# Optimization experiments

Measured on AMD Instinct MI355X. Metric: run time of the kernel, lower is better.

The kernel has to match this reference:

```python
import jax, jax.numpy as jnp
import numpy as np

N, E, H = 40000, 320000, 128
T = 4                      # towers
F_IN = H // T              # 32, divide_input=True
F_OUT = H // T             # 32
NUM_AGG, NUM_SCALER = 5, 3


def _lin(k, out_d, in_d):
    return jax.random.normal(k, (out_d, in_d), jnp.float32) / np.sqrt(in_d)


def setup_inputs() -> dict:
    key = jax.random.key(0)
    ks = jax.random.split(key, 16)
    inp = {}
    inp["atom_x"] = jax.random.normal(ks[0], (N, H), jnp.float32)
    inp["bond_x"] = jax.random.randint(ks[1], (E,), 0, 5)
    inp["atom_edge_index"] = jax.random.randint(ks[2], (2, E), 0, N)
    inp["deg_hist"] = jnp.ones((17,), jnp.int32)
    # bond embedding table (Embedding(5, H))
    inp["emb"] = jax.random.normal(ks[3], (5, H), jnp.float32)
    # edge_encoder: Linear(edge_dim=H, F_IN)
    inp["edge_w"] = _lin(ks[4], F_IN, H)
    inp["edge_b"] = jnp.zeros((F_IN,), jnp.float32)
    # pre_nns per tower: Linear(3F,F) -> ReLU -> Linear(F,F)
    inp["pre_w0"] = jax.random.normal(ks[5], (T, F_IN, 3 * F_IN), jnp.float32) / np.sqrt(3 * F_IN)
    inp["pre_b0"] = jnp.zeros((T, F_IN), jnp.float32)
    inp["pre_w1"] = jax.random.normal(ks[6], (T, F_IN, F_IN), jnp.float32) / np.sqrt(F_IN)
    inp["pre_b1"] = jnp.zeros((T, F_IN), jnp.float32)
    # post_nns per tower: Linear((5*3+1)F, F) -> ReLU -> Linear(F,F)
    post_in = (NUM_AGG * NUM_SCALER + 1) * F_IN
    inp["post_w0"] = jax.random.normal(ks[7], (T, F_OUT, post_in), jnp.float32) / np.sqrt(post_in)
    inp["post_b0"] = jnp.zeros((T, F_OUT), jnp.float32)
    inp["post_w1"] = jax.random.normal(ks[8], (T, F_OUT, F_OUT), jnp.float32) / np.sqrt(F_OUT)
    inp["post_b1"] = jnp.zeros((T, F_OUT), jnp.float32)
    # final Linear(H, H)
    inp["lin_w"] = _lin(ks[9], H, H)
    inp["lin_b"] = jnp.zeros((H,), jnp.float32)
    # LayerNorm(H)
    inp["ln_g"] = jnp.ones((H,), jnp.float32)
    inp["ln_b"] = jnp.zeros((H,), jnp.float32)
    return inp


def _pna_forward(atom_x, bond_emb, src, dst, deg_hist,
                 edge_w, edge_b, pre_w0, pre_b0, pre_w1, pre_b1,
                 post_w0, post_b0, post_w1, post_b1, lin_w, lin_b, ln_g, ln_b):
    n = atom_x.shape[0]
    x = atom_x.reshape(n, T, F_IN)                       # divide_input
    # message: cat([x_i, x_j, edge_attr]) per tower, then per-tower pre-MLP
    e = bond_emb @ edge_w.T + edge_b                     # [E, F_IN]
    e = jnp.broadcast_to(e[:, None, :], (e.shape[0], T, F_IN))
    h = jnp.concatenate([x[dst], x[src], e], axis=-1)    # [E, T, 3F]
    h = jnp.einsum('etf,tgf->etg', h, pre_w0) + pre_b0
    h = jnp.einsum('etf,tgf->etg', jax.nn.relu(h), pre_w1) + pre_b1  # [E, T, F]

    # 5 scatter aggregations over destination nodes
    cnt = jax.ops.segment_sum(jnp.ones((h.shape[0],), h.dtype), dst, n)   # in-degree
    cnt1 = jnp.maximum(cnt, 1.0)[:, None, None]
    s = jax.ops.segment_sum(h, dst, n)
    mean = s / cnt1
    mean2 = jax.ops.segment_sum(h * h, dst, n) / cnt1
    std = jnp.sqrt(jax.nn.relu(mean2 - mean * mean) + 1e-5)
    has = (cnt > 0)[:, None, None]
    mn = jnp.where(has, jax.ops.segment_min(h, dst, n), 0.0)
    mx = jnp.where(has, jax.ops.segment_max(h, dst, n), 0.0)
    agg = jnp.concatenate([s, mean, mn, mx, std], axis=-1)  # [N, T, 5F]

    # degree scalers: identity / amplification / attenuation
    dh = deg_hist.astype(jnp.float32)
    bins = jnp.arange(dh.shape[0], dtype=jnp.float32)
    avg_log = jnp.sum(jnp.log(bins + 1.0) * dh) / jnp.sum(dh)
    logd = jnp.log(cnt1 + 1.0)                            # deg clamped to >=1
    agg = jnp.concatenate([agg, agg * (logd / avg_log), agg * (avg_log / logd)], axis=-1)  # [N,T,15F]

    # post-MLP per tower on cat([x, agg])
    out = jnp.concatenate([x, agg], axis=-1)              # [N, T, 16F]
    out = jnp.einsum('ntf,tgf->ntg', out, post_w0) + post_b0
    out = jnp.einsum('ntf,tgf->ntg', jax.nn.relu(out), post_w1) + post_b1
    out = out.reshape(n, T * F_OUT) @ lin_w.T + lin_b     # [N, H]

    # LayerNorm -> ReLU -> residual (dropout is identity in eval)
    mu = out.mean(-1, keepdims=True)
    var = ((out - mu) ** 2).mean(-1, keepdims=True)
    out = (out - mu) / jnp.sqrt(var + 1e-5) * ln_g + ln_b
    return atom_x + jax.nn.relu(out)


def reference(atom_x, bond_x, atom_edge_index, deg_hist, emb, edge_w, edge_b,
              pre_w0, pre_b0, pre_w1, pre_b1, post_w0, post_b0, post_w1, post_b1,
              lin_w, lin_b, ln_g, ln_b):
    src, dst = atom_edge_index[0], atom_edge_index[1]
    bond_emb = emb[bond_x]                                # Embedding(5, H)
    return _pna_forward(atom_x, bond_emb, src, dst, deg_hist,
                        edge_w, edge_b, pre_w0, pre_b0, pre_w1, pre_b1,
                        post_w0, post_b0, post_w1, post_b1, lin_w, lin_b, ln_g, ln_b)
```

## Files before the change

kernel.cpp:

```cpp
#include <hip/hip_runtime.h>
#include <hip/hip_fp16.h>
#include <math.h>

#define T_TOW 4
#define F_DIM 32
#define H_DIM 128

typedef _Float16 half2_t __attribute__((ext_vector_type(2)));

#if defined(__has_builtin)
#if __has_builtin(__builtin_amdgcn_fdot2)
#define HAVE_FDOT2 1
#endif
#endif

static __device__ __forceinline__ float fdot2_acc(half2_t a, half2_t b, float c) {
#ifdef HAVE_FDOT2
    return __builtin_amdgcn_fdot2(a, b, c, false);
#else
    return c + (float)a.x * (float)b.x + (float)a.y * (float)b.y;
#endif
}

static __device__ __forceinline__ half2_t u2h(unsigned u) {
    union { unsigned u; half2_t h; } x; x.u = u; return x.h;
}
static __device__ __forceinline__ unsigned h2u(float a, float b) {
    union { half2_t h; unsigned u; } x;
    x.h.x = (_Float16)a; x.h.y = (_Float16)b; return x.u;
}

__global__ void k_setup(const float* __restrict__ emb, const float* __restrict__ edge_w,
                        const float* __restrict__ edge_b, const float* __restrict__ pre_w0,
                        const float* __restrict__ pre_b0, const int* __restrict__ deg_hist,
                        float* __restrict__ ctab, float* __restrict__ scal) {
    __shared__ float e_sh[5 * 32];
    int tid = threadIdx.x;
    for (int i = tid; i < 5 * 32; i += blockDim.x) {
        int b = i >> 5, f = i & 31;
        float acc = edge_b[f];
        const float* er = emb + b * 128;
        const float* wr = edge_w + f * 128;
        for (int k = 0; k < 128; ++k) acc += er[k] * wr[k];
        e_sh[i] = acc;
    }
    __syncthreads();
    for (int i = tid; i < 5 * 128; i += blockDim.x) {
        int b = i >> 7, c = i & 127;
        float acc = pre_b0[c];
        const float* w = pre_w0 + c * 96 + 64;
        const float* e = e_sh + b * 32;
        for (int f = 0; f < 32; ++f) acc += w[f] * e[f];
        ctab[i] = acc;
    }
    if (tid == 0) {
        float num = 0.f, den = 0.f;
        for (int i = 0; i < 17; ++i) {
            float d = (float)deg_hist[i];
            num += logf((float)(i + 1)) * d;
            den += d;
        }
        scal[0] = num / den;
    }
}

__global__ void k_transpose2(const float* __restrict__ post_w0, const float* __restrict__ post_w1,
                             const float* __restrict__ lin_w, const float* __restrict__ pre_w0,
                             unsigned* __restrict__ W3h, float* __restrict__ w1t,
                             float* __restrict__ lwt, float* __restrict__ wab) {
    int i = blockIdx.x * blockDim.x + threadIdx.x;
    if (i < T_TOW * 3 * 96 * 32) {
        int t = i / (3 * 96 * 32);
        int r = i % (3 * 96 * 32);
        int p = r / (96 * 32);
        int r2 = r % (96 * 32);
        int k2 = r2 >> 5, g = r2 & 31;
        const float* row = post_w0 + (size_t)(t * 32 + g) * 512;
        float v0, v1;
        int k0 = 2 * k2, k1 = 2 * k2 + 1;
        if (p == 0) { v0 = row[k0]; v1 = row[k1]; }
        else {
            v0 = (k0 >= 32) ? row[p * 160 + k0] : 0.f;
            v1 = (k1 >= 32) ? row[p * 160 + k1] : 0.f;
        }
        W3h[i] = h2u(v0, v1);
    }
    if (i < T_TOW * F_DIM * F_DIM) {
        int t = i >> 10;
        int r = i & 1023;
        int g = r >> 5, f = r & 31;
        w1t[(t * 32 + f) * 32 + g] = post_w1[i];
    }
    if (i < H_DIM * H_DIM) {
        int j = i >> 7, k = i & 127;
        lwt[k * H_DIM + j] = lin_w[i];
    }
    if (i < 2 * T_TOW * F_DIM * F_DIM) {
        int s = i >> 12;
        int r = i & 4095;
        int t = r >> 10;
        int r2 = r & 1023;
        int f = r2 >> 5, g = r2 & 31;
        wab[i] = pre_w0[(size_t)(t * 32 + g) * 96 + s * 32 + f];
    }
}

__global__ void k_count(const int* __restrict__ dst, int* __restrict__ cnt, int E) {
    int e = blockIdx.x * blockDim.x + threadIdx.x;
    if (e < E) atomicAdd(&cnt[dst[e]], 1);
}

__global__ void k_blocksum(const int* __restrict__ cnt, int* __restrict__ bsum, int n) {
    __shared__ int sh[256];
    int i = blockIdx.x * 256 + threadIdx.x;
    sh[threadIdx.x] = (i < n) ? cnt[i] : 0;
    __syncthreads();
    for (int off = 128; off > 0; off >>= 1) {
        if (threadIdx.x < off) sh[threadIdx.x] += sh[threadIdx.x + off];
        __syncthreads();
    }
    if (threadIdx.x == 0) bsum[blockIdx.x] = sh[0];
}

__global__ void k_scanb(const int* __restrict__ bsum, int* __restrict__ boff, int nb,
                        int* __restrict__ rs, int n_nodes) {
    __shared__ int sh[512];
    int tid = threadIdx.x;
    int v = (tid < nb) ? bsum[tid] : 0;
    sh[tid] = v;
    __syncthreads();
    for (int off = 1; off < 512; off <<= 1) {
        int u = (tid >= off) ? sh[tid - off] : 0;
        __syncthreads();
        sh[tid] += u;
        __syncthreads();
    }
    if (tid < nb) boff[tid] = sh[tid] - v;
    if (tid == 511) rs[n_nodes] = sh[511];
}

__global__ void k_scanc(const int* __restrict__ cnt, const int* __restrict__ boff,
                        int* __restrict__ rs, int* __restrict__ cur, int n) {
    __shared__ int sh[256];
    int i = blockIdx.x * 256 + threadIdx.x;
    int v = (i < n) ? cnt[i] : 0;
    sh[threadIdx.x] = v;
    __syncthreads();
    for (int off = 1; off < 256; off <<= 1) {
        int u = (threadIdx.x >= off) ? sh[threadIdx.x - off] : 0;
        __syncthreads();
        sh[threadIdx.x] += u;
        __syncthreads();
    }
    if (i < n) {
        int excl = sh[threadIdx.x] - v + boff[blockIdx.x];
        rs[i] = excl;
        cur[i] = excl;
    }
}

__global__ void k_bucket(const int* __restrict__ src, const int* __restrict__ dst,
                         const int* __restrict__ bond, int* __restrict__ cur,
                         int* __restrict__ srcS, int* __restrict__ bndS, int E) {
    int e = blockIdx.x * blockDim.x + threadIdx.x;
    if (e < E) {
        int d = dst[e];
        int slot = atomicAdd(&cur[d], 1);
        srcS[slot] = src[e];
        bndS[slot] = bond[e];
    }
}

__global__ __launch_bounds__(256) void k_ab3(
    const float* __restrict__ x, const float* __restrict__ wab,
    float* __restrict__ A, _Float16* __restrict__ Bh, int n) {
    __shared__ float xt[64 * 133];
    int tid = threadIdx.x;
    int base = blockIdx.x * 64;
    for (int i = tid; i < 2048; i += 256) {
        int nl = i >> 5, q = i & 31;
        int node = min(base + nl, n - 1);
        float4 v = *(const float4*)(x + (size_t)node * 128 + q * 4);
        float* d = xt + nl * 133 + q * 4;
        d[0] = v.x; d[1] = v.y; d[2] = v.z; d[3] = v.w;
    }
    __syncthreads();
    int t = __builtin_amdgcn_readfirstlane(tid >> 6);
    int lane = tid & 63;
    float accA[32], accB[32];
#pragma unroll
    for (int g = 0; g < 32; ++g) { accA[g] = 0.f; accB[g] = 0.f; }
    const float* xs = xt + lane * 133 + t * 32;
    const float* wa = wab + (size_t)t * 1024;
    const float* wb = wab + 4096 + (size_t)t * 1024;
    for (int f = 0; f < 32; ++f) {
        float v = xs[f];
#pragma unroll
        for (int g = 0; g < 32; ++g) {
            accA[g] += wa[g] * v;
            accB[g] += wb[g] * v;
        }
        wa += 32; wb += 32;
    }
    int node = base + lane;
    if (node < n) {
        float* ar = A + (size_t)node * 128 + t * 32;
#pragma unroll
        for (int q = 0; q < 8; ++q)
            *(float4*)(ar + q * 4) = make_float4(accA[q * 4], accA[q * 4 + 1], accA[q * 4 + 2], accA[q * 4 + 3]);
        _Float16* br = Bh + (size_t)node * 128 + t * 32;
#pragma unroll
        for (int q = 0; q < 4; ++q) {
            uint4 u;
            u.x = h2u(accB[8 * q + 0], accB[8 * q + 1]);
            u.y = h2u(accB[8 * q + 2], accB[8 * q + 3]);
            u.z = h2u(accB[8 * q + 4], accB[8 * q + 5]);
            u.w = h2u(accB[8 * q + 6], accB[8 * q + 7]);
            *(uint4*)(br + q * 8) = u;
        }
    }
}

__global__ __launch_bounds__(256, 4) void k_edge7(
    const float* __restrict__ A, const _Float16* __restrict__ Bh,
    const float* __restrict__ ctab, const float* __restrict__ pre_w1,
    const float* __restrict__ pre_b1, const int* __restrict__ rs,
    const int* __restrict__ srcS, const int* __restrict__ bndS,
    float* __restrict__ stats, int n) {
    __shared__ _Float16 w1h[128 * 33];
    __shared__ float cbuf[640];
    __shared__ unsigned pbuf[4][64];
    int tid = threadIdx.x;
    for (int i = tid; i < 4096; i += 256) w1h[(i >> 5) * 33 + (i & 31)] = (_Float16)pre_w1[i];
    for (int i = tid; i < 640; i += 256) cbuf[i] = ctab[i];
    __syncthreads();

    int w = tid >> 6;
    int lane = tid & 63;
    int node = blockIdx.x * 4 + w;
    if (node >= n) return;
    int c0 = lane * 2;
    int t = lane >> 4;
    int i16 = lane & 15;

    half2_t wpa[16], wpb[16];
    {
        const _Float16* ra = w1h + c0 * 33;
        const _Float16* rb = w1h + (c0 + 1) * 33;
#pragma unroll
        for (int j = 0; j < 16; ++j) {
            wpa[j].x = ra[2 * j]; wpa[j].y = ra[2 * j + 1];
            wpb[j].x = rb[2 * j]; wpb[j].y = rb[2 * j + 1];
        }
    }
    float b1a = pre_b1[c0], b1b = pre_b1[c0 + 1];
    float2 av = ((const float2*)(A + (size_t)node * H_DIM))[lane];
    const uint4* pk4 = (const uint4*)&pbuf[w][t * 16];
    unsigned* pslot = &pbuf[w][t * 16 + i16];

    int e0 = rs[node], e1 = rs[node + 1];
    float sum0 = 0.f, sum1 = 0.f, sq0 = 0.f, sq1 = 0.f;
    float mn0 = INFINITY, mn1 = INFINITY, mx0 = -INFINITY, mx1 = -INFINITY;

    half2_t b2_n; b2_n.x = (_Float16)0.f; b2_n.y = (_Float16)0.f;
    float2 c2_n = make_float2(0.f, 0.f);
    if (e0 < e1) {
        int sv = srcS[e0];
        int bv = bndS[e0];
        b2_n = ((const half2_t*)(Bh + (size_t)sv * H_DIM))[lane];
        c2_n = ((const float2*)(cbuf + bv * 128))[lane];
    }
    for (int e = e0; e < e1; ++e) {
        half2_t b2 = b2_n;
        float2 c2 = c2_n;
        if (e + 1 < e1) {
            int sv = srcS[e + 1];
            int bv = bndS[e + 1];
            b2_n = ((const half2_t*)(Bh + (size_t)sv * H_DIM))[lane];
            c2_n = ((const float2*)(cbuf + bv * 128))[lane];
        }
        float p0 = fmaxf(av.x + (float)b2.x + c2.x, 0.f);
        float p1 = fmaxf(av.y + (float)b2.y + c2.y, 0.f);
        *pslot = h2u(p0, p1);
        float hx = b1a, hy = b1b;
#pragma unroll
        for (int q = 0; q < 4; ++q) {
            uint4 v = pk4[q];
            hx = fdot2_acc(wpa[4 * q + 0], u2h(v.x), hx);
            hy = fdot2_acc(wpb[4 * q + 0], u2h(v.x), hy);
            hx = fdot2_acc(wpa[4 * q + 1], u2h(v.y), hx);
            hy = fdot2_acc(wpb[4 * q + 1], u2h(v.y), hy);
            hx = fdot2_acc(wpa[4 * q + 2], u2h(v.z), hx);
            hy = fdot2_acc(wpb[4 * q + 2], u2h(v.z), hy);
            hx = fdot2_acc(wpa[4 * q + 3], u2h(v.w), hx);
            hy = fdot2_acc(wpb[4 * q + 3], u2h(v.w), hy);
        }
        sum0 += hx; sum1 += hy;
        sq0 += hx * hx; sq1 += hy * hy;
        mn0 = fminf(mn0, hx); mn1 = fminf(mn1, hy);
        mx0 = fmaxf(mx0, hx); mx1 = fmaxf(mx1, hy);
    }
    if (e1 <= e0) { mn0 = mn1 = mx0 = mx1 = 0.f; }
    float2* st2 = (float2*)(stats + (size_t)node * 512);
    st2[lane]        = make_float2(sum0, sum1);
    st2[64 + lane]   = make_float2(sq0, sq1);
    st2[128 + lane]  = make_float2(mn0, mn1);
    st2[192 + lane]  = make_float2(mx0, mx1);
}

__global__ __launch_bounds__(192) void k_post5(
    const float* __restrict__ x, const float* __restrict__ stats,
    const int* __restrict__ rs, const float* __restrict__ scal,
    const unsigned* __restrict__ W3h, const float* __restrict__ w1t,
    const float* __restrict__ post_b0, const float* __restrict__ post_b1,
    __half* __restrict__ y1, int n) {
    __shared__ __align__(16) char smraw[64 * 194 * 2];
    __half* uh = (__half*)smraw;
    __half* zh = (__half*)smraw;
    __half* rh = (__half*)(smraw + 3 * 64 * 34 * 2);
    int bid = blockIdx.x;
    int tile = bid >> 2, t = bid & 3;
    int tid = threadIdx.x;
    int p = __builtin_amdgcn_readfirstlane(tid >> 6);
    int lane = tid & 63;
    int base = tile * 64;

    for (int i = tid; i < 512; i += 192) {
        int nl = i >> 3, q = i & 7;
        int node = min(base + nl, n - 1);
        float4 v = *(const float4*)(x + (size_t)node * 128 + t * 32 + q * 4);
        __half* d = uh + nl * 194 + q * 4;
        d[0] = __float2half(v.x); d[1] = __float2half(v.y);
        d[2] = __float2half(v.z); d[3] = __float2half(v.w);
    }
    for (int i = tid; i < 512; i += 192) {
        int nl = i >> 3, q = i & 7;
        int node = min(base + nl, n - 1);
        int cnt = rs[node + 1] - rs[node];
        float inv = 1.f / fmaxf((float)cnt, 1.f);
        const float* sp = stats + (size_t)node * 512 + t * 32 + q * 4;
        float4 s4  = *(const float4*)(sp);
        float4 q4  = *(const float4*)(sp + 128);
        float4 mn4 = *(const float4*)(sp + 256);
        float4 mx4 = *(const float4*)(sp + 384);
        float me[4] = { s4.x * inv, s4.y * inv, s4.z * inv, s4.w * inv };
        float qq[4] = { q4.x, q4.y, q4.z, q4.w };
        __half* d = uh + nl * 194 + q * 4;
        d[32] = __float2half(s4.x);  d[33] = __float2half(s4.y);
        d[34] = __float2half(s4.z);  d[35] = __float2half(s4.w);
#pragma unroll
        for (int j = 0; j < 4; ++j) {
            d[64 + j] = __float2half(me[j]);
            d[160 + j] = __float2half(sqrtf(fmaxf(qq[j] * inv - me[j] * me[j], 0.f) + 1e-5f));
        }
        d[96] = __float2half(mn4.x);  d[97] = __float2half(mn4.y);
        d[98] = __float2half(mn4.z);  d[99] = __float2half(mn4.w);
        d[128] = __float2half(mx4.x); d[129] = __float2half(mx4.y);
        d[130] = __float2half(mx4.z); d[131] = __float2half(mx4.w);
    }
    __syncthreads();

    float acc[32];
#pragma unroll
    for (int g = 0; g < 32; ++g) acc[g] = 0.f;
    int k20 = (p == 0) ? 0 : 16;
    const unsigned* wrow = W3h + ((size_t)(t * 3 + p) * 96 + k20) * 32;
    const unsigned* us2 = (const unsigned*)(uh + lane * 194);
    for (int k2 = k20; k2 < 96; ++k2) {
        half2_t uv = u2h(us2[k2]);
#pragma unroll
        for (int g = 0; g < 32; ++g) acc[g] = fdot2_acc(u2h(wrow[g]), uv, acc[g]);
        wrow += 32;
    }
    __syncthreads();
    {
        __half* zb = zh + p * (64 * 34) + lane * 34;
#pragma unroll
        for (int g = 0; g < 32; ++g) zb[g] = __float2half(acc[g]);
    }
    __syncthreads();
    if (tid < 64) {
        int nodec = min(base + tid, n - 1);
        int cnt = rs[nodec + 1] - rs[nodec];
        float cnt1 = fmaxf((float)cnt, 1.f);
        float logd = logf(cnt1 + 1.f);
        float avg = scal[0];
        float s1 = logd / avg, s2 = avg / logd;
        const float* b0 = post_b0 + t * 32;
        const __half* z0 = zh + tid * 34;
        const __half* z1 = zh + 64 * 34 + tid * 34;
        const __half* z2 = zh + 2 * 64 * 34 + tid * 34;
        __half* rb = rh + tid * 34;
#pragma unroll
        for (int g = 0; g < 32; ++g) {
            float r = __half2float(z0[g]) + s1 * __half2float(z1[g]) + s2 * __half2float(z2[g]) + b0[g];
            rb[g] = __float2half(fmaxf(r, 0.f));
        }
    }
    __syncthreads();
    if (tid < 128) {
        int h = __builtin_amdgcn_readfirstlane(tid >> 6);
        int l = tid & 63;
        float acc2[16];
        const float* b1 = post_b1 + t * 32 + h * 16;
#pragma unroll
        for (int j = 0; j < 16; ++j) acc2[j] = b1[j];
        const __half* rb = rh + l * 34;
        const float* w1 = w1t + (t * 32) * 32 + h * 16;
#pragma unroll
        for (int f = 0; f < 32; ++f) {
            float rv = __half2float(rb[f]);
#pragma unroll
            for (int j = 0; j < 16; ++j) acc2[j] += w1[f * 32 + j] * rv;
        }
        int node2 = base + l;
        if (node2 < n) {
            __half* yr = y1 + (size_t)node2 * 128 + t * 32 + h * 16;
#pragma unroll
            for (int j = 0; j < 16; ++j) yr[j] = __float2half(acc2[j]);
        }
    }
}

__global__ __launch_bounds__(256) void k_final3(
    const __half* __restrict__ y1, const float* __restrict__ lwt,
    const float* __restrict__ lin_b, const float* __restrict__ ln_g,
    const float* __restrict__ ln_b, const float* __restrict__ x,
    float* __restrict__ out, int n) {
    __shared__ __half yt[64 * 130];
    __shared__ float lnbuf[64][8];
    int tid = threadIdx.x;
    int base = blockIdx.x * 64;
    for (int i = tid; i < 1024; i += 256) {
        int nl = i >> 4, q = i & 15;
        int node = min(base + nl, n - 1);
        const __half* sp = y1 + (size_t)node * 128 + q * 8;
        __half* d = yt + nl * 130 + q * 8;
#pragma unroll
        for (int j = 0; j < 8; ++j) d[j] = sp[j];
    }
    __syncthreads();
    int w = __builtin_amdgcn_readfirstlane(tid >> 6);
    int l = tid & 63;
    int j0 = w * 32;
    float acc[32];
    const float* lb = lin_b + j0;
#pragma unroll
    for (int j = 0; j < 32; ++j) acc[j] = lb[j];
    const __half* yrow = yt + l * 130;
    const float* wr = lwt + j0;
    for (int k = 0; k < 128; ++k) {
        float v = __half2float(yrow[k]);
#pragma unroll
        for (int j = 0; j < 32; ++j) acc[j] += wr[j] * v;
        wr += 128;
    }
    float s = 0.f, sq = 0.f;
#pragma unroll
    for (int j = 0; j < 32; ++j) { s += acc[j]; sq += acc[j] * acc[j]; }
    lnbuf[l][w * 2] = s;
    lnbuf[l][w * 2 + 1] = sq;
    __syncthreads();
    float S = 0.f, SQ = 0.f;
#pragma unroll
    for (int i = 0; i < 4; ++i) { S += lnbuf[l][2 * i]; SQ += lnbuf[l][2 * i + 1]; }
    float mu = S * (1.f / 128.f);
    float var = fmaxf(SQ * (1.f / 128.f) - mu * mu, 0.f);
    float rstd = rsqrtf(var + 1e-5f);
    int node = base + l;
    if (node < n) {
        const float* xr = x + (size_t)node * 128 + j0;
        float* orow = out + (size_t)node * 128 + j0;
#pragma unroll
        for (int j = 0; j < 32; ++j) {
            float o = (acc[j] - mu) * rstd * ln_g[j0 + j] + ln_b[j0 + j];
            orow[j] = xr[j] + fmaxf(o, 0.f);
        }
    }
}

extern "C" void kernel_launch(void* const* d_in, const int* in_sizes, int n_in,
                              void* d_out, int out_size, void* d_ws, size_t ws_size,
                              hipStream_t stream) {
    const float* atom_x   = (const float*)d_in[0];
    const int*   bond_x   = (const int*)d_in[1];
    const int*   aei      = (const int*)d_in[2];
    const int*   deg_hist = (const int*)d_in[3];
    const float* emb      = (const float*)d_in[4];
    const float* edge_w   = (const float*)d_in[5];
    const float* edge_b   = (const float*)d_in[6];
    const float* pre_w0   = (const float*)d_in[7];
    const float* pre_b0   = (const float*)d_in[8];
    const float* pre_w1   = (const float*)d_in[9];
    const float* pre_b1   = (const float*)d_in[10];
    const float* post_w0  = (const float*)d_in[11];
    const float* post_b0  = (const float*)d_in[12];
    const float* post_w1  = (const float*)d_in[13];
    const float* post_b1  = (const float*)d_in[14];
    const float* lin_w    = (const float*)d_in[15];
    const float* lin_b    = (const float*)d_in[16];
    const float* ln_g     = (const float*)d_in[17];
    const float* ln_b     = (const float*)d_in[18];

    int n = in_sizes[0] / H_DIM;
    int E = in_sizes[1];
    const int* src = aei;
    const int* dst = aei + E;

    char* ws = (char*)d_ws;
    size_t off = 0;
    auto alloc = [&](size_t bytes) {
        size_t r = off;
        off = (off + bytes + 511) & ~(size_t)511;
        return r;
    };
    float*    ctab  = (float*)(ws + alloc(5 * 128 * 4));
    float*    scal  = (float*)(ws + alloc(256));
    unsigned* W3h   = (unsigned*)(ws + alloc((size_t)4 * 3 * 96 * 32 * 4));
    float*    w1t   = (float*)(ws + alloc(4 * 32 * 32 * 4));
    float*    lwt   = (float*)(ws + alloc(128 * 128 * 4));
    float*    wab   = (float*)(ws + alloc(2 * 4 * 32 * 32 * 4));
    int*      cnt   = (int*)(ws + alloc((size_t)n * 4));
    int*      rs    = (int*)(ws + alloc((size_t)(n + 1) * 4));
    int*      cur   = (int*)(ws + alloc((size_t)n * 4));
    int*      bsum  = (int*)(ws + alloc(4096));
    int*      boff  = (int*)(ws + alloc(4096));
    int*      srcS  = (int*)(ws + alloc((size_t)E * 4));
    int*      bndS  = (int*)(ws + alloc((size_t)E * 4));
    float*    A     = (float*)(ws + alloc((size_t)n * 128 * 4));
    _Float16* Bh    = (_Float16*)(ws + alloc((size_t)n * 128 * 2));
    float*    stats = (float*)(ws + alloc((size_t)n * 512 * 4));
    __half*   y1    = (__half*)A;

    if (off > ws_size) return;

    hipMemsetAsync(cnt, 0, (size_t)n * 4, stream);
    k_setup<<<1, 256, 0, stream>>>(emb, edge_w, edge_b, pre_w0, pre_b0, deg_hist, ctab, scal);
    k_transpose2<<<(T_TOW * 3 * 96 * 32 + 255) / 256, 256, 0, stream>>>(post_w0, post_w1, lin_w,
                                                                        pre_w0, W3h, w1t, lwt, wab);
    k_count<<<(E + 255) / 256, 256, 0, stream>>>(dst, cnt, E);
    int nb = (n + 255) / 256;
    k_blocksum<<<nb, 256, 0, stream>>>(cnt, bsum, n);
    k_scanb<<<1, 512, 0, stream>>>(bsum, boff, nb, rs, n);
    k_scanc<<<nb, 256, 0, stream>>>(cnt, boff, rs, cur, n);
    k_bucket<<<(E + 255) / 256, 256, 0, stream>>>(src, dst, bond_x, cur, srcS, bndS, E);
    int nTiles = (n + 63) / 64;
    k_ab3<<<nTiles, 256, 0, stream>>>(atom_x, wab, A, Bh, n);
    k_edge7<<<(n + 3) / 4, 256, 0, stream>>>(A, Bh, ctab, pre_w1, pre_b1, rs, srcS, bndS,
                                             stats, n);
    k_post5<<<nTiles * 4, 192, 0, stream>>>(atom_x, stats, rs, scal, W3h, w1t,
                                            post_b0, post_b1, y1, n);
    k_final3<<<nTiles, 256, 0, stream>>>(y1, lwt, lin_b, ln_g, ln_b, atom_x,
                                         (float*)d_out, n);
}
```

Before: 264.2 us.

## Merge setup kernels, single-block scan, and prepacked pre_w1 for edge kernel

Fuses the setup, transpose and degree-count kernels into a single prep kernel, and replaces the three-kernel CSR scan with one 1024-thread block scan, cutting the launch count. The edge kernel now loads pre_w1 pre-packed in fp16 from global memory with uint4 loads instead of staging it through shared memory. That frees shared memory, so occupancy is requested at 8 blocks per CU. The trade-offs are a serial per-thread chunk scan in a single block and atomics now concentrated in fewer blocks.

```diff
diff --git a/kernel.cpp b/kernel.cpp
--- a/kernel.cpp
+++ b/kernel.cpp
@@ -30,45 +30,47 @@
     x.h.x = (_Float16)a; x.h.y = (_Float16)b; return x.u;
 }
 
-__global__ void k_setup(const float* __restrict__ emb, const float* __restrict__ edge_w,
-                        const float* __restrict__ edge_b, const float* __restrict__ pre_w0,
-                        const float* __restrict__ pre_b0, const int* __restrict__ deg_hist,
-                        float* __restrict__ ctab, float* __restrict__ scal) {
-    __shared__ float e_sh[5 * 32];
-    int tid = threadIdx.x;
-    for (int i = tid; i < 5 * 32; i += blockDim.x) {
-        int b = i >> 5, f = i & 31;
-        float acc = edge_b[f];
-        const float* er = emb + b * 128;
-        const float* wr = edge_w + f * 128;
-        for (int k = 0; k < 128; ++k) acc += er[k] * wr[k];
-        e_sh[i] = acc;
-    }
-    __syncthreads();
-    for (int i = tid; i < 5 * 128; i += blockDim.x) {
-        int b = i >> 7, c = i & 127;
-        float acc = pre_b0[c];
-        const float* w = pre_w0 + c * 96 + 64;
-        const float* e = e_sh + b * 32;
-        for (int f = 0; f < 32; ++f) acc += w[f] * e[f];
-        ctab[i] = acc;
-    }
-    if (tid == 0) {
-        float num = 0.f, den = 0.f;
-        for (int i = 0; i < 17; ++i) {
-            float d = (float)deg_hist[i];
-            num += logf((float)(i + 1)) * d;
-            den += d;
-        }
-        scal[0] = num / den;
-    }
-}
-
-__global__ void k_transpose2(const float* __restrict__ post_w0, const float* __restrict__ post_w1,
-                             const float* __restrict__ lin_w, const float* __restrict__ pre_w0,
-                             unsigned* __restrict__ W3h, float* __restrict__ w1t,
-                             float* __restrict__ lwt, float* __restrict__ wab) {
+__global__ void k_prep(const float* __restrict__ emb, const float* __restrict__ edge_w,
+                       const float* __restrict__ edge_b, const float* __restrict__ pre_w0,
+                       const float* __restrict__ pre_b0, const float* __restrict__ pre_w1,
+                       const int* __restrict__ deg_hist,
+                       const float* __restrict__ post_w0, const float* __restrict__ post_w1,
+                       const float* __restrict__ lin_w, const int* __restrict__ dst, int E,
+                       float* __restrict__ ctab, float* __restrict__ scal,
+                       unsigned* __restrict__ W3h, float* __restrict__ w1t,
+                       float* __restrict__ lwt, float* __restrict__ wab,
+                       unsigned* __restrict__ w1q, int* __restrict__ cnt) {
     int i = blockIdx.x * blockDim.x + threadIdx.x;
+    if (blockIdx.x == 0) {
+        __shared__ float e_sh[5 * 32];
+        int tid = threadIdx.x;
+        for (int j = tid; j < 5 * 32; j += blockDim.x) {
+            int b = j >> 5, f = j & 31;
+            float acc = edge_b[f];
+            const float* er = emb + b * 128;
+            const float* wr = edge_w + f * 128;
+            for (int k = 0; k < 128; ++k) acc += er[k] * wr[k];
+            e_sh[j] = acc;
+        }
+        __syncthreads();
+        for (int j = tid; j < 5 * 128; j += blockDim.x) {
+            int b = j >> 7, c = j & 127;
+            float acc = pre_b0[c];
+            const float* w = pre_w0 + c * 96 + 64;
+            const float* e = e_sh + b * 32;
+            for (int f = 0; f < 32; ++f) acc += w[f] * e[f];
+            ctab[j] = acc;
+        }
+        if (tid == 0) {
+            float num = 0.f, den = 0.f;
+            for (int j = 0; j < 17; ++j) {
+                float d = (float)deg_hist[j];
+                num += logf((float)(j + 1)) * d;
+                den += d;
+            }
+            scal[0] = num / den;
+        }
+    }
     if (i < T_TOW * 3 * 96 * 32) {
         int t = i / (3 * 96 * 32);
         int r = i % (3 * 96 * 32);
@@ -103,60 +105,40 @@
         int f = r2 >> 5, g = r2 & 31;
         wab[i] = pre_w0[(size_t)(t * 32 + g) * 96 + s * 32 + f];
     }
-}
-
-__global__ void k_count(const int* __restrict__ dst, int* __restrict__ cnt, int E) {
-    int e = blockIdx.x * blockDim.x + threadIdx.x;
-    if (e < E) atomicAdd(&cnt[dst[e]], 1);
-}
-
-__global__ void k_blocksum(const int* __restrict__ cnt, int* __restrict__ bsum, int n) {
-    __shared__ int sh[256];
-    int i = blockIdx.x * 256 + threadIdx.x;
-    sh[threadIdx.x] = (i < n) ? cnt[i] : 0;
-    __syncthreads();
-    for (int off = 128; off > 0; off >>= 1) {
-        if (threadIdx.x < off) sh[threadIdx.x] += sh[threadIdx.x + off];
-        __syncthreads();
-    }
-    if (threadIdx.x == 0) bsum[blockIdx.x] = sh[0];
-}
-
-__global__ void k_scanb(const int* __restrict__ bsum, int* __restrict__ boff, int nb,
-                        int* __restrict__ rs, int n_nodes) {
-    __shared__ int sh[512];
+    if (i < 2048) {
+        int q = i >> 8;
+        int lane = (i >> 2) & 63;
+        int s = i & 3;
+        int j = (q < 4) ? 4 * q + s : 4 * (q - 4) + s;
+        int c = (q < 4) ? 2 * lane : 2 * lane + 1;
+        w1q[i] = h2u(pre_w1[c * 32 + 2 * j], pre_w1[c * 32 + 2 * j + 1]);
+    }
+    for (int e = i; e < E; e += gridDim.x * blockDim.x) atomicAdd(&cnt[dst[e]], 1);
+}
+
+__global__ __launch_bounds__(1024) void k_scan_all(const int* __restrict__ cnt,
+                                                   int* __restrict__ rs,
+                                                   int* __restrict__ cur, int n) {
+    __shared__ int sh[1024];
     int tid = threadIdx.x;
-    int v = (tid < nb) ? bsum[tid] : 0;
-    sh[tid] = v;
-    __syncthreads();
-    for (int off = 1; off < 512; off <<= 1) {
+    int chunk = (n + 1023) >> 10;
+    int c0 = tid * chunk, c1 = min(c0 + chunk, n);
+    int s = 0;
+    for (int j = c0; j < c1; ++j) s += cnt[j];
+    sh[tid] = s;
+    __syncthreads();
+    for (int off = 1; off < 1024; off <<= 1) {
         int u = (tid >= off) ? sh[tid - off] : 0;
         __syncthreads();
         sh[tid] += u;
         __syncthreads();
     }
-    if (tid < nb) boff[tid] = sh[tid] - v;
-    if (tid == 511) rs[n_nodes] = sh[511];
-}
-
-__global__ void k_scanc(const int* __restrict__ cnt, const int* __restrict__ boff,
-                        int* __restrict__ rs, int* __restrict__ cur, int n) {
-    __shared__ int sh[256];
-    int i = blockIdx.x * 256 + threadIdx.x;
-    int v = (i < n) ? cnt[i] : 0;
-    sh[threadIdx.x] = v;
-    __syncthreads();
-    for (int off = 1; off < 256; off <<= 1) {
-        int u = (threadIdx.x >= off) ? sh[threadIdx.x - off] : 0;
-        __syncthreads();
-        sh[threadIdx.x] += u;
-        __syncthreads();
-    }
-    if (i < n) {
-        int excl = sh[threadIdx.x] - v + boff[blockIdx.x];
-        rs[i] = excl;
-        cur[i] = excl;
-    }
+    int run = sh[tid] - s;
+    for (int j = c0; j < c1; ++j) {
+        rs[j] = run; cur[j] = run;
+        run += cnt[j];
+    }
+    if (tid == 1023) rs[n] = sh[1023];
 }
 
 __global__ void k_bucket(const int* __restrict__ src, const int* __restrict__ dst,
@@ -221,17 +203,15 @@
     }
 }
 
-__global__ __launch_bounds__(256, 4) void k_edge7(
+__global__ __launch_bounds__(256, 8) void k_edge8(
     const float* __restrict__ A, const _Float16* __restrict__ Bh,
-    const float* __restrict__ ctab, const float* __restrict__ pre_w1,
+    const float* __restrict__ ctab, const unsigned* __restrict__ w1q,
     const float* __restrict__ pre_b1, const int* __restrict__ rs,
     const int* __restrict__ srcS, const int* __restrict__ bndS,
     float* __restrict__ stats, int n) {
-    __shared__ _Float16 w1h[128 * 33];
     __shared__ float cbuf[640];
     __shared__ unsigned pbuf[4][64];
     int tid = threadIdx.x;
-    for (int i = tid; i < 4096; i += 256) w1h[(i >> 5) * 33 + (i & 31)] = (_Float16)pre_w1[i];
     for (int i = tid; i < 640; i += 256) cbuf[i] = ctab[i];
     __syncthreads();
 
@@ -245,12 +225,18 @@
 
     half2_t wpa[16], wpb[16];
     {
-        const _Float16* ra = w1h + c0 * 33;
-        const _Float16* rb = w1h + (c0 + 1) * 33;
-#pragma unroll
-        for (int j = 0; j < 16; ++j) {
-            wpa[j].x = ra[2 * j]; wpa[j].y = ra[2 * j + 1];
-            wpb[j].x = rb[2 * j]; wpb[j].y = rb[2 * j + 1];
+        const uint4* wq = (const uint4*)w1q;
+#pragma unroll
+        for (int q = 0; q < 4; ++q) {
+            uint4 v = wq[q * 64 + lane];
+            wpa[4 * q + 0] = u2h(v.x); wpa[4 * q + 1] = u2h(v.y);
+            wpa[4 * q + 2] = u2h(v.z); wpa[4 * q + 3] = u2h(v.w);
+        }
+#pragma unroll
+        for (int q = 0; q < 4; ++q) {
+            uint4 v = wq[(q + 4) * 64 + lane];
+            wpb[4 * q + 0] = u2h(v.x); wpb[4 * q + 1] = u2h(v.y);
+            wpb[4 * q + 2] = u2h(v.z); wpb[4 * q + 3] = u2h(v.w);
         }
     }
     float b1a = pre_b1[c0], b1b = pre_b1[c0 + 1];
@@ -520,11 +506,10 @@
     float*    w1t   = (float*)(ws + alloc(4 * 32 * 32 * 4));
     float*    lwt   = (float*)(ws + alloc(128 * 128 * 4));
     float*    wab   = (float*)(ws + alloc(2 * 4 * 32 * 32 * 4));
+    unsigned* w1q   = (unsigned*)(ws + alloc(2048 * 4));
     int*      cnt   = (int*)(ws + alloc((size_t)n * 4));
     int*      rs    = (int*)(ws + alloc((size_t)(n + 1) * 4));
     int*      cur   = (int*)(ws + alloc((size_t)n * 4));
-    int*      bsum  = (int*)(ws + alloc(4096));
-    int*      boff  = (int*)(ws + alloc(4096));
     int*      srcS  = (int*)(ws + alloc((size_t)E * 4));
     int*      bndS  = (int*)(ws + alloc((size_t)E * 4));
     float*    A     = (float*)(ws + alloc((size_t)n * 128 * 4));
@@ -535,18 +520,15 @@
     if (off > ws_size) return;
 
     hipMemsetAsync(cnt, 0, (size_t)n * 4, stream);
-    k_setup<<<1, 256, 0, stream>>>(emb, edge_w, edge_b, pre_w0, pre_b0, deg_hist, ctab, scal);
-    k_transpose2<<<(T_TOW * 3 * 96 * 32 + 255) / 256, 256, 0, stream>>>(post_w0, post_w1, lin_w,
-                                                                        pre_w0, W3h, w1t, lwt, wab);
-    k_count<<<(E + 255) / 256, 256, 0, stream>>>(dst, cnt, E);
-    int nb = (n + 255) / 256;
-    k_blocksum<<<nb, 256, 0, stream>>>(cnt, bsum, n);
-    k_scanb<<<1, 512, 0, stream>>>(bsum, boff, nb, rs, n);
-    k_scanc<<<nb, 256, 0, stream>>>(cnt, boff, rs, cur, n);
+    int nPrep = (T_TOW * 3 * 96 * 32 + 255) / 256;
+    k_prep<<<nPrep, 256, 0, stream>>>(emb, edge_w, edge_b, pre_w0, pre_b0, pre_w1, deg_hist,
+                                      post_w0, post_w1, lin_w, dst, E,
+                                      ctab, scal, W3h, w1t, lwt, wab, w1q, cnt);
+    k_scan_all<<<1, 1024, 0, stream>>>(cnt, rs, cur, n);
     k_bucket<<<(E + 255) / 256, 256, 0, stream>>>(src, dst, bond_x, cur, srcS, bndS, E);
     int nTiles = (n + 63) / 64;
     k_ab3<<<nTiles, 256, 0, stream>>>(atom_x, wab, A, Bh, n);
-    k_edge7<<<(n + 3) / 4, 256, 0, stream>>>(A, Bh, ctab, pre_w1, pre_b1, rs, srcS, bndS,
+    k_edge8<<<(n + 3) / 4, 256, 0, stream>>>(A, Bh, ctab, w1q, pre_b1, rs, srcS, bndS,
                                              stats, n);
     k_post5<<<nTiles * 4, 192, 0, stream>>>(atom_x, stats, rs, scal, W3h, w1t,
                                             post_b0, post_b1, y1, n);
```

Result: slower. 317.1 us (+20.0%).
